# Kernel optimization log

Hardware: AMD Instinct MI355X
Metric: run time of the kernel (lower is better)

The kernel has to match this reference:

```python
import jax, jax.numpy as jnp
import numpy as np

B, S, H = 4, 2048, 1024
E, I, K = 8, 2048, 2


def setup_inputs() -> dict:
    key = jax.random.key(0)
    ks = jax.random.split(key, 6)
    return {
        "hidden_states": jax.random.normal(ks[0], (B, S, H), dtype=jnp.float32),
        "Wg": jax.random.normal(ks[1], (H, E), dtype=jnp.float32) * 0.02,
        "W1": jax.random.normal(ks[2], (E, H, I), dtype=jnp.float32) * 0.02,
        "b1": jnp.zeros((E, I), dtype=jnp.float32),
        "W2": jax.random.normal(ks[3], (E, I, H), dtype=jnp.float32) * 0.02,
        "b2": jnp.zeros((E, H), dtype=jnp.float32),
    }


def reference(hidden_states, Wg, W1, b1, W2, b2):
    b, s, h = hidden_states.shape
    x = hidden_states.reshape(-1, h)                      # [T, H]
    gate_logits = x @ Wg                                  # [T, E]
    gate_probs = jax.nn.softmax(gate_logits, axis=-1)
    topk_probs, topk_idx = jax.lax.top_k(gate_probs, K)   # [T, K]
    topk_probs = topk_probs / jnp.sum(topk_probs, axis=-1, keepdims=True)
    # dense combine weights [T, E] (zero where expert not selected)
    T = x.shape[0]
    w = jnp.zeros((T, E), dtype=x.dtype)
    w = w.at[jnp.arange(T)[:, None], topk_idx].set(topk_probs)
    # run every expert on all tokens (dense grouped-GEMM form), exact erf GELU
    h1 = jax.nn.gelu(jnp.einsum('th,ehi->eti', x, W1) + b1[:, None, :], approximate=False)  # [E, T, I]
    y = jnp.einsum('eti,eih->eth', h1, W2) + b2[:, None, :]                                  # [E, T, H]
    out = jnp.einsum('te,eth->th', w, y)                                                     # [T, H]
    return out.reshape(b, s, h)
```

## Files before the change

kernel.cpp:

```cpp
#include <hip/hip_runtime.h>
#include <math.h>

#define TOKS 8192
#define HD 1024
#define ID 2048
#define NE 8

typedef __bf16 bf16_t;
typedef __bf16 bf16x8 __attribute__((ext_vector_type(8)));
typedef float f32x4 __attribute__((ext_vector_type(4)));

#define GLOAD(gp, lp)                                                \
  __builtin_amdgcn_global_load_lds(                                  \
      (const __attribute__((address_space(1))) void*)(gp),           \
      (__attribute__((address_space(3))) void*)(lp), 16, 0, 0)

#define WAITV(N) asm volatile("s_waitcnt vmcnt(" #N ")" ::: "memory")
#define WAITL0() asm volatile("s_waitcnt lgkmcnt(0)" ::: "memory")

__device__ __forceinline__ float gelu_exact(float v) {
  const float u = v * 0.70710678118654752f;
  const float a = fabsf(u);
  const float t = 1.f / (1.f + 0.3275911f * a);
  const float poly =
      t * (0.254829592f +
           t * (-0.284496736f +
                t * (1.421413741f + t * (-1.453152027f + t * 1.061405429f))));
  float er = 1.f - poly * __expf(-a * a);
  er = copysignf(er, u);
  return 0.5f * v * (1.f + er);
}

#define WS_COUNTS 0
#define WS_OFFSETS 32
#define WS_BTOK 128
#define WS_BW (128 + 65536)
#define WS_TE (128 + 2 * 65536)
#define WS_TW (128 + 3 * 65536)
#define WS_WL 263168ull
#define WS_BLKC 266240ull
#define WS_BLKB 270336ull
#define WS_POS 274432ull
#define WS_XB 524288ull
#define WS_H1 (WS_XB + 16777216ull)
#define WS_WT (WS_H1 + 67108864ull)
#define WS_Y (WS_WT + 33554432ull)

#define MAXWL 144
#define BM 128

__global__ __launch_bounds__(256) void gate_kernel(const float* __restrict__ x,
                                                   const float* __restrict__ Wg,
                                                   bf16_t* __restrict__ xb,
                                                   int* __restrict__ tok_e,
                                                   float* __restrict__ tok_w) {
  __shared__ float WgT[NE][HD];
  const int tid = threadIdx.x;
#pragma unroll
  for (int i = 0; i < NE * HD / 256; ++i) {
    const int idx = i * 256 + tid;
    WgT[idx & 7][idx >> 3] = Wg[idx];
  }
  __syncthreads();
  const int wv = tid >> 6;
  const int lane = tid & 63;
#pragma unroll
  for (int s = 0; s < 2; ++s) {
    const int t = blockIdx.x * 8 + wv * 2 + s;
    const float* xrow = x + (size_t)t * HD;
    bf16_t* xbrow = xb + (size_t)t * HD;
    float acc[NE];
#pragma unroll
    for (int e = 0; e < NE; ++e) acc[e] = 0.f;
#pragma unroll
    for (int i = 0; i < 16; ++i) {
      const int h = i * 64 + lane;
      const float xv = xrow[h];
      xbrow[h] = (bf16_t)xv;
#pragma unroll
      for (int e = 0; e < NE; ++e) acc[e] += xv * WgT[e][h];
    }
#pragma unroll
    for (int off = 32; off >= 1; off >>= 1) {
#pragma unroll
      for (int e = 0; e < NE; ++e) acc[e] += __shfl_xor(acc[e], off);
    }
    if (lane == 0) {
      int i1 = 0;
      float l1 = acc[0];
#pragma unroll
      for (int e = 1; e < NE; ++e)
        if (acc[e] > l1) { l1 = acc[e]; i1 = e; }
      int i2 = -1;
      float l2 = -3.4e38f;
#pragma unroll
      for (int e = 0; e < NE; ++e)
        if (e != i1 && acc[e] > l2) { l2 = acc[e]; i2 = e; }
      const float q = expf(l2 - l1);
      const float w1 = 1.f / (1.f + q);
      tok_e[2 * t] = i1;
      tok_e[2 * t + 1] = i2;
      tok_w[2 * t] = w1;
      tok_w[2 * t + 1] = q * w1;
    }
  }
}

__global__ __launch_bounds__(256) void hist_kernel(const int* __restrict__ tok_e,
                                                   int* __restrict__ blk_cnt) {
  __shared__ int wcnt[4][NE];
  const int tid = threadIdx.x;
  const int idx = blockIdx.x * 256 + tid;
  const int e = tok_e[idx];
  const int w = tid >> 6;
  const int lane = tid & 63;
#pragma unroll
  for (int e0 = 0; e0 < NE; ++e0) {
    const unsigned long long m = __ballot(e == e0);
    if (lane == 0) wcnt[w][e0] = __popcll(m);
  }
  __syncthreads();
  if (tid < NE)
    blk_cnt[blockIdx.x * NE + tid] =
        wcnt[0][tid] + wcnt[1][tid] + wcnt[2][tid] + wcnt[3][tid];
}

__global__ void scan_kernel(const int* __restrict__ blk_cnt, int* __restrict__ counts,
                            int* __restrict__ offsets, int* __restrict__ blk_base,
                            int* __restrict__ wl_e, int* __restrict__ wl_m,
                            int* __restrict__ n_work) {
  const int b = threadIdx.x;
  int c[NE], pre[NE], tot[NE];
#pragma unroll
  for (int e = 0; e < NE; ++e) c[e] = blk_cnt[b * NE + e];
#pragma unroll
  for (int e = 0; e < NE; ++e) {
    int v = c[e];
#pragma unroll
    for (int off = 1; off < 64; off <<= 1) {
      const int u = __shfl_up(v, off);
      if (b >= off) v += u;
    }
    pre[e] = v - c[e];
    tot[e] = __shfl(v, 63);
  }
  int off_[NE];
  int s = 0;
#pragma unroll
  for (int e = 0; e < NE; ++e) {
    off_[e] = s;
    s += tot[e];
  }
#pragma unroll
  for (int e = 0; e < NE; ++e) blk_base[b * NE + e] = off_[e] + pre[e];
  if (b == 0) {
    int idx = 0;
    for (int e = 0; e < NE; ++e) {
      counts[e] = tot[e];
      offsets[e] = off_[e];
      for (int m = 0; m < tot[e] && idx < MAXWL; m += BM) {
        wl_e[idx] = e;
        wl_m[idx] = m;
        ++idx;
      }
    }
    *n_work = idx;
  }
}

__global__ __launch_bounds__(256) void scatter_kernel(const int* __restrict__ tok_e,
                                                      const float* __restrict__ tok_w,
                                                      const int* __restrict__ blk_base,
                                                      int* __restrict__ bucket_tok,
                                                      float* __restrict__ bucket_w,
                                                      int* __restrict__ pos_of) {
  __shared__ int wcnt[4][NE];
  const int tid = threadIdx.x;
  const int idx = blockIdx.x * 256 + tid;
  const int e = tok_e[idx];
  const int w = tid >> 6;
  const int lane = tid & 63;
  unsigned long long mym = 0;
#pragma unroll
  for (int e0 = 0; e0 < NE; ++e0) {
    const unsigned long long m = __ballot(e == e0);
    if (lane == 0) wcnt[w][e0] = __popcll(m);
    if (e0 == e) mym = m;
  }
  __syncthreads();
  int base = blk_base[blockIdx.x * NE + e];
  for (int w2 = 0; w2 < w; ++w2) base += wcnt[w2][e];
  const int rank = __popcll(mym & ((1ull << lane) - 1ull));
  const int pos = base + rank;
  bucket_tok[pos] = idx >> 1;
  bucket_w[pos] = tok_w[idx];
  pos_of[idx] = pos;
}

__global__ __launch_bounds__(256) void transpose_convert_kernel(const float* __restrict__ src,
                                                                bf16_t* __restrict__ dst, int K,
                                                                int N) {
  __shared__ float tile[64][65];
  const int e = blockIdx.z;
  const int k0 = blockIdx.x * 64;
  const int n0 = blockIdx.y * 64;
  const float* s = src + (size_t)e * K * N;
  bf16_t* d = dst + (size_t)e * K * N;
  const int t = threadIdx.x;
  const int c4 = (t & 15) * 4;
  const int rr = t >> 4;
#pragma unroll
  for (int p = 0; p < 4; ++p) {
    const int r = p * 16 + rr;
    const float4 v = *(const float4*)(s + (size_t)(k0 + r) * N + n0 + c4);
    tile[r][c4] = v.x;
    tile[r][c4 + 1] = v.y;
    tile[r][c4 + 2] = v.z;
    tile[r][c4 + 3] = v.w;
  }
  __syncthreads();
  const int kc = t & 7;
  const int nb = t >> 3;
#pragma unroll
  for (int p = 0; p < 2; ++p) {
    const int n = p * 32 + nb;
    bf16_t o[8];
#pragma unroll
    for (int j = 0; j < 8; ++j) o[j] = (bf16_t)tile[kc * 8 + j][n];
    *(uint4*)(d + (size_t)(n0 + n) * K + k0 + kc * 8) = *(uint4*)o;
  }
}


__global__ __launch_bounds__(256, 3) void gemm1_kernel(
    const bf16_t* __restrict__ xb, const bf16_t* __restrict__ W1T, const float* __restrict__ b1,
    const int* __restrict__ counts, const int* __restrict__ offsets,
    const int* __restrict__ bucket_tok, const int* __restrict__ wl_e,
    const int* __restrict__ wl_m, const int* __restrict__ n_work, bf16_t* __restrict__ h1) {
  const int widx = blockIdx.x;
  if (widx >= *n_work) return;
  const int e = wl_e[widx];
  const int m_base = wl_m[widx];
  const int n_e = counts[e];
  const int n_base = blockIdx.y * 128;
  const int off = offsets[e];

  __shared__ bf16_t As[3][128 * 32];
  __shared__ bf16_t Bs[3][128 * 32];

  const int tid = threadIdx.x;
  const int w = tid >> 6;
  const int lane = tid & 63;
  const int quad = lane >> 4;
  const int lrow = lane & 15;
  const int wm = w >> 1;
  const int wn = w & 1;

  const int srow = lane >> 2;
  const int kch = (((lane & 3) ^ ((lane >> 4) & 3)) * 8);
  int r0 = m_base + w * 32 + srow;
  int r1 = r0 + 16;
  if (r0 >= n_e) r0 = n_e - 1;
  if (r1 >= n_e) r1 = n_e - 1;
  const bf16_t* ga0 = xb + (size_t)bucket_tok[off + r0] * HD + kch;
  const bf16_t* ga1 = xb + (size_t)bucket_tok[off + r1] * HD + kch;
  const bf16_t* gb0 = W1T + ((size_t)e * ID + n_base + w * 32 + srow) * HD + kch;
  const bf16_t* gb1 = gb0 + (size_t)16 * HD;
  const int laofs0 = w * 1024 + lane * 8;
  const int laofs1 = laofs0 + 512;

  f32x4 acc[4][4];
#pragma unroll
  for (int mt = 0; mt < 4; ++mt)
#pragma unroll
    for (int nt = 0; nt < 4; ++nt)
#pragma unroll
      for (int r = 0; r < 4; ++r) acc[mt][nt][r] = 0.f;

#pragma unroll
  for (int p = 0; p < 2; ++p) {
    const size_t ko = (size_t)p * 32;
    GLOAD(ga0 + ko, &As[p][laofs0]);
    GLOAD(ga1 + ko, &As[p][laofs1]);
    GLOAD(gb0 + ko, &Bs[p][laofs0]);
    GLOAD(gb1 + ko, &Bs[p][laofs1]);
  }

  const int slot = (quad ^ ((lrow >> 2) & 3)) * 8;
  int cur = 0;
  int pre = 2;
#define NT1 (HD / 32)
  for (int kt = 0; kt < NT1; ++kt) {
    WAITL0();
    __builtin_amdgcn_s_barrier();
    if (kt + 2 < NT1) {
      const size_t ko = (size_t)(kt + 2) * 32;
      GLOAD(ga0 + ko, &As[pre][laofs0]);
      GLOAD(ga1 + ko, &As[pre][laofs1]);
      GLOAD(gb0 + ko, &Bs[pre][laofs0]);
      GLOAD(gb1 + ko, &Bs[pre][laofs1]);
      WAITV(8);
    } else if (kt + 1 < NT1) {
      WAITV(4);
    } else {
      WAITV(0);
    }
    __builtin_amdgcn_s_barrier();
    __builtin_amdgcn_sched_barrier(0);
    bf16x8 af[4], bfr[4];
#pragma unroll
    for (int i = 0; i < 4; ++i) {
      af[i] = *(const bf16x8*)(&As[cur][(wm * 64 + i * 16 + lrow) * 32 + slot]);
      bfr[i] = *(const bf16x8*)(&Bs[cur][(wn * 64 + i * 16 + lrow) * 32 + slot]);
    }
#pragma unroll
    for (int mt = 0; mt < 4; ++mt)
#pragma unroll
      for (int nt = 0; nt < 4; ++nt)
        acc[mt][nt] =
            __builtin_amdgcn_mfma_f32_16x16x32_bf16(bfr[nt], af[mt], acc[mt][nt], 0, 0, 0);
    cur = (cur == 2) ? 0 : cur + 1;
    pre = (pre == 2) ? 0 : pre + 1;
  }

#pragma unroll
  for (int mt = 0; mt < 4; ++mt) {
    const int gm = m_base + wm * 64 + mt * 16 + lrow;
    if (gm < n_e) {
      bf16_t* orow = h1 + (size_t)(off + gm) * ID;
#pragma unroll
      for (int nt = 0; nt < 4; ++nt) {
        const int gi0 = n_base + wn * 64 + nt * 16 + quad * 4;
        const float4 bb = *(const float4*)(b1 + e * ID + gi0);
        const float bv[4] = {bb.x, bb.y, bb.z, bb.w};
        bf16_t o[4];
#pragma unroll
        for (int r = 0; r < 4; ++r) o[r] = (bf16_t)gelu_exact(acc[mt][nt][r] + bv[r]);
        *(uint2*)(orow + gi0) = *(uint2*)o;
      }
    }
  }
}

__global__ __launch_bounds__(256, 3) void gemm2_kernel(
    const bf16_t* __restrict__ h1, const bf16_t* __restrict__ W2T, const float* __restrict__ b2,
    const int* __restrict__ counts, const int* __restrict__ offsets,
    const int* __restrict__ wl_e, const int* __restrict__ wl_m, const int* __restrict__ n_work,
    bf16_t* __restrict__ y) {
  const int widx = blockIdx.x;
  if (widx >= *n_work) return;
  const int e = wl_e[widx];
  const int m_base = wl_m[widx];
  const int n_e = counts[e];
  const int n_base = blockIdx.y * 128;
  const int off = offsets[e];

  __shared__ bf16_t As[3][128 * 32];
  __shared__ bf16_t Bs[3][128 * 32];

  const int tid = threadIdx.x;
  const int w = tid >> 6;
  const int lane = tid & 63;
  const int quad = lane >> 4;
  const int lrow = lane & 15;
  const int wm = w >> 1;
  const int wn = w & 1;

  const int srow = lane >> 2;
  const int kch = (((lane & 3) ^ ((lane >> 4) & 3)) * 8);
  int r0 = m_base + w * 32 + srow;
  int r1 = r0 + 16;
  if (r0 >= n_e) r0 = n_e - 1;
  if (r1 >= n_e) r1 = n_e - 1;
  const bf16_t* ga0 = h1 + (size_t)(off + r0) * ID + kch;
  const bf16_t* ga1 = h1 + (size_t)(off + r1) * ID + kch;
  const bf16_t* gb0 = W2T + ((size_t)e * HD + n_base + w * 32 + srow) * ID + kch;
  const bf16_t* gb1 = gb0 + (size_t)16 * ID;
  const int laofs0 = w * 1024 + lane * 8;
  const int laofs1 = laofs0 + 512;

  f32x4 acc[4][4];
#pragma unroll
  for (int mt = 0; mt < 4; ++mt)
#pragma unroll
    for (int nt = 0; nt < 4; ++nt)
#pragma unroll
      for (int r = 0; r < 4; ++r) acc[mt][nt][r] = 0.f;

#pragma unroll
  for (int p = 0; p < 2; ++p) {
    const size_t ko = (size_t)p * 32;
    GLOAD(ga0 + ko, &As[p][laofs0]);
    GLOAD(ga1 + ko, &As[p][laofs1]);
    GLOAD(gb0 + ko, &Bs[p][laofs0]);
    GLOAD(gb1 + ko, &Bs[p][laofs1]);
  }

  const int slot = (quad ^ ((lrow >> 2) & 3)) * 8;
  int cur = 0;
  int pre = 2;
#define NT2 (ID / 32)
  for (int kt = 0; kt < NT2; ++kt) {
    WAITL0();
    __builtin_amdgcn_s_barrier();
    if (kt + 2 < NT2) {
      const size_t ko = (size_t)(kt + 2) * 32;
      GLOAD(ga0 + ko, &As[pre][laofs0]);
      GLOAD(ga1 + ko, &As[pre][laofs1]);
      GLOAD(gb0 + ko, &Bs[pre][laofs0]);
      GLOAD(gb1 + ko, &Bs[pre][laofs1]);
      WAITV(8);
    } else if (kt + 1 < NT2) {
      WAITV(4);
    } else {
      WAITV(0);
    }
    __builtin_amdgcn_s_barrier();
    __builtin_amdgcn_sched_barrier(0);
    bf16x8 af[4], bfr[4];
#pragma unroll
    for (int i = 0; i < 4; ++i) {
      af[i] = *(const bf16x8*)(&As[cur][(wm * 64 + i * 16 + lrow) * 32 + slot]);
      bfr[i] = *(const bf16x8*)(&Bs[cur][(wn * 64 + i * 16 + lrow) * 32 + slot]);
    }
#pragma unroll
    for (int mt = 0; mt < 4; ++mt)
#pragma unroll
      for (int nt = 0; nt < 4; ++nt)
        acc[mt][nt] =
            __builtin_amdgcn_mfma_f32_16x16x32_bf16(bfr[nt], af[mt], acc[mt][nt], 0, 0, 0);
    cur = (cur == 2) ? 0 : cur + 1;
    pre = (pre == 2) ? 0 : pre + 1;
  }

#pragma unroll
  for (int mt = 0; mt < 4; ++mt) {
    const int gm = m_base + wm * 64 + mt * 16 + lrow;
    if (gm < n_e) {
      bf16_t* orow = y + (size_t)(off + gm) * HD;
#pragma unroll
      for (int nt = 0; nt < 4; ++nt) {
        const int gi0 = n_base + wn * 64 + nt * 16 + quad * 4;
        const float4 bb = *(const float4*)(b2 + e * HD + gi0);
        const float bv[4] = {bb.x, bb.y, bb.z, bb.w};
        bf16_t o[4];
#pragma unroll
        for (int r = 0; r < 4; ++r) o[r] = (bf16_t)(acc[mt][nt][r] + bv[r]);
        *(uint2*)(orow + gi0) = *(uint2*)o;
      }
    }
  }
}

__global__ __launch_bounds__(256) void combine_kernel(const bf16_t* __restrict__ y,
                                                      const int* __restrict__ pos_of,
                                                      const float* __restrict__ tok_w,
                                                      float* __restrict__ out) {
  const int gid = blockIdx.x * 256 + threadIdx.x;
  const int t = gid >> 7;
  const int c8 = (gid & 127) * 8;
  const int p1 = pos_of[2 * t];
  const int p2 = pos_of[2 * t + 1];
  const float w1 = tok_w[2 * t];
  const float w2 = tok_w[2 * t + 1];
  const bf16x8 a = *(const bf16x8*)(y + (size_t)p1 * HD + c8);
  const bf16x8 b = *(const bf16x8*)(y + (size_t)p2 * HD + c8);
  float* op = out + (size_t)t * HD + c8;
  float ov[8];
#pragma unroll
  for (int j = 0; j < 8; ++j) ov[j] = w1 * (float)a[j] + w2 * (float)b[j];
  *(float4*)op = make_float4(ov[0], ov[1], ov[2], ov[3]);
  *(float4*)(op + 4) = make_float4(ov[4], ov[5], ov[6], ov[7]);
}

extern "C" void kernel_launch(void* const* d_in, const int* in_sizes, int n_in,
                              void* d_out, int out_size, void* d_ws, size_t ws_size,
                              hipStream_t stream) {
  const float* x = (const float*)d_in[0];
  const float* Wg = (const float*)d_in[1];
  const float* W1 = (const float*)d_in[2];
  const float* b1 = (const float*)d_in[3];
  const float* W2 = (const float*)d_in[4];
  const float* b2 = (const float*)d_in[5];
  float* out = (float*)d_out;
  char* ws = (char*)d_ws;

  int* counts = (int*)(ws + WS_COUNTS);
  int* offsets = (int*)(ws + WS_OFFSETS);
  int* bucket_tok = (int*)(ws + WS_BTOK);
  float* bucket_w = (float*)(ws + WS_BW);
  int* tok_e = (int*)(ws + WS_TE);
  float* tok_w = (float*)(ws + WS_TW);
  int* wl_e = (int*)(ws + WS_WL);
  int* wl_m = wl_e + MAXWL;
  int* n_work = wl_m + MAXWL;
  int* blk_cnt = (int*)(ws + WS_BLKC);
  int* blk_base = (int*)(ws + WS_BLKB);
  int* pos_of = (int*)(ws + WS_POS);
  bf16_t* xb = (bf16_t*)(ws + WS_XB);
  bf16_t* h1 = (bf16_t*)(ws + WS_H1);
  bf16_t* WT = (bf16_t*)(ws + WS_WT);
  bf16_t* y = (bf16_t*)(ws + WS_Y);

  gate_kernel<<<TOKS / 8, 256, 0, stream>>>(x, Wg, xb, tok_e, tok_w);
  hist_kernel<<<TOKS * 2 / 256, 256, 0, stream>>>(tok_e, blk_cnt);
  scan_kernel<<<1, 64, 0, stream>>>(blk_cnt, counts, offsets, blk_base, wl_e, wl_m, n_work);
  scatter_kernel<<<TOKS * 2 / 256, 256, 0, stream>>>(tok_e, tok_w, blk_base, bucket_tok,
                                                     bucket_w, pos_of);
  transpose_convert_kernel<<<dim3(HD / 64, ID / 64, NE), 256, 0, stream>>>(W1, WT, HD, ID);
  gemm1_kernel<<<dim3(MAXWL, ID / 128), 256, 0, stream>>>(xb, WT, b1, counts, offsets, bucket_tok,
                                                          wl_e, wl_m, n_work, h1);
  transpose_convert_kernel<<<dim3(ID / 64, HD / 64, NE), 256, 0, stream>>>(W2, WT, ID, HD);
  gemm2_kernel<<<dim3(MAXWL, HD / 128), 256, 0, stream>>>(h1, WT, b2, counts, offsets, wl_e,
                                                          wl_m, n_work, y);
  combine_kernel<<<TOKS * HD / (256 * 8), 256, 0, stream>>>(y, pos_of, tok_w, out);
}
```

Measured before the change: 447.8 us.

## Fuse expert histogram into gate kernel, vectorize gate weights, raise MFMA priority

The gate kernel now counts per-block expert assignments with shared-memory atomics and records each slot's local rank, which removes the separate histogram kernel launch. The scan kernel is extended to handle 1024 gate blocks (16 per lane), and the scatter kernel uses the precomputed ranks in place of ballots. Gate weights are kept in their natural [H,E] layout and read as float4 pairs. The GEMM inner loops also wrap the MFMA block in s_setprio to favour the math waves. Atomic ranks make bucket order within an expert nondeterministic, and the scan does more serial work per thread.

```diff
diff --git a/kernel.cpp b/kernel.cpp
--- a/kernel.cpp
+++ b/kernel.cpp
@@ -38,9 +38,10 @@
 #define WS_TE (128 + 2 * 65536)
 #define WS_TW (128 + 3 * 65536)
 #define WS_WL 263168ull
-#define WS_BLKC 266240ull
-#define WS_BLKB 270336ull
 #define WS_POS 274432ull
+#define WS_RANK 339968ull
+#define WS_BLKC 405504ull
+#define WS_BLKB 438272ull
 #define WS_XB 524288ull
 #define WS_H1 (WS_XB + 16777216ull)
 #define WS_WT (WS_H1 + 67108864ull)
@@ -48,19 +49,24 @@
 
 #define MAXWL 144
 #define BM 128
+#define GB (TOKS / 8)
 
 __global__ __launch_bounds__(256) void gate_kernel(const float* __restrict__ x,
                                                    const float* __restrict__ Wg,
                                                    bf16_t* __restrict__ xb,
                                                    int* __restrict__ tok_e,
-                                                   float* __restrict__ tok_w) {
-  __shared__ float WgT[NE][HD];
+                                                   float* __restrict__ tok_w,
+                                                   int* __restrict__ rank_of,
+                                                   int* __restrict__ blk_cnt) {
+  __shared__ float WgT[HD * NE];
+  __shared__ int cnt[NE];
   const int tid = threadIdx.x;
 #pragma unroll
-  for (int i = 0; i < NE * HD / 256; ++i) {
-    const int idx = i * 256 + tid;
-    WgT[idx & 7][idx >> 3] = Wg[idx];
-  }
+  for (int i = 0; i < NE * HD / (256 * 4); ++i) {
+    const int k = i * 256 + tid;
+    ((float4*)WgT)[k] = ((const float4*)Wg)[k];
+  }
+  if (tid < NE) cnt[tid] = 0;
   __syncthreads();
   const int wv = tid >> 6;
   const int lane = tid & 63;
@@ -77,8 +83,16 @@
       const int h = i * 64 + lane;
       const float xv = xrow[h];
       xbrow[h] = (bf16_t)xv;
-#pragma unroll
-      for (int e = 0; e < NE; ++e) acc[e] += xv * WgT[e][h];
+      const float4 w0 = *(const float4*)(WgT + h * NE);
+      const float4 w1 = *(const float4*)(WgT + h * NE + 4);
+      acc[0] += xv * w0.x;
+      acc[1] += xv * w0.y;
+      acc[2] += xv * w0.z;
+      acc[3] += xv * w0.w;
+      acc[4] += xv * w1.x;
+      acc[5] += xv * w1.y;
+      acc[6] += xv * w1.z;
+      acc[7] += xv * w1.w;
     }
 #pragma unroll
     for (int off = 32; off >= 1; off >>= 1) {
@@ -102,27 +116,12 @@
       tok_e[2 * t + 1] = i2;
       tok_w[2 * t] = w1;
       tok_w[2 * t + 1] = q * w1;
-    }
-  }
-}
-
-__global__ __launch_bounds__(256) void hist_kernel(const int* __restrict__ tok_e,
-                                                   int* __restrict__ blk_cnt) {
-  __shared__ int wcnt[4][NE];
-  const int tid = threadIdx.x;
-  const int idx = blockIdx.x * 256 + tid;
-  const int e = tok_e[idx];
-  const int w = tid >> 6;
-  const int lane = tid & 63;
-#pragma unroll
-  for (int e0 = 0; e0 < NE; ++e0) {
-    const unsigned long long m = __ballot(e == e0);
-    if (lane == 0) wcnt[w][e0] = __popcll(m);
+      rank_of[2 * t] = atomicAdd(&cnt[i1], 1);
+      rank_of[2 * t + 1] = atomicAdd(&cnt[i2], 1);
+    }
   }
   __syncthreads();
-  if (tid < NE)
-    blk_cnt[blockIdx.x * NE + tid] =
-        wcnt[0][tid] + wcnt[1][tid] + wcnt[2][tid] + wcnt[3][tid];
+  if (tid < NE) blk_cnt[blockIdx.x * NE + tid] = cnt[tid];
 }
 
 __global__ void scan_kernel(const int* __restrict__ blk_cnt, int* __restrict__ counts,
@@ -130,18 +129,22 @@
                             int* __restrict__ wl_e, int* __restrict__ wl_m,
                             int* __restrict__ n_work) {
   const int b = threadIdx.x;
-  int c[NE], pre[NE], tot[NE];
-#pragma unroll
-  for (int e = 0; e < NE; ++e) c[e] = blk_cnt[b * NE + e];
+  int sum[NE], pre[NE], tot[NE];
 #pragma unroll
   for (int e = 0; e < NE; ++e) {
-    int v = c[e];
+    int s = 0;
+    for (int j = 0; j < 16; ++j) s += blk_cnt[(b * 16 + j) * NE + e];
+    sum[e] = s;
+  }
+#pragma unroll
+  for (int e = 0; e < NE; ++e) {
+    int v = sum[e];
 #pragma unroll
     for (int off = 1; off < 64; off <<= 1) {
       const int u = __shfl_up(v, off);
       if (b >= off) v += u;
     }
-    pre[e] = v - c[e];
+    pre[e] = v - sum[e];
     tot[e] = __shfl(v, 63);
   }
   int off_[NE];
@@ -152,7 +155,13 @@
     s += tot[e];
   }
 #pragma unroll
-  for (int e = 0; e < NE; ++e) blk_base[b * NE + e] = off_[e] + pre[e];
+  for (int e = 0; e < NE; ++e) {
+    int run = off_[e] + pre[e];
+    for (int j = 0; j < 16; ++j) {
+      blk_base[(b * 16 + j) * NE + e] = run;
+      run += blk_cnt[(b * 16 + j) * NE + e];
+    }
+  }
   if (b == 0) {
     int idx = 0;
     for (int e = 0; e < NE; ++e) {
@@ -171,27 +180,14 @@
 __global__ __launch_bounds__(256) void scatter_kernel(const int* __restrict__ tok_e,
                                                       const float* __restrict__ tok_w,
                                                       const int* __restrict__ blk_base,
+                                                      const int* __restrict__ rank_of,
                                                       int* __restrict__ bucket_tok,
                                                       float* __restrict__ bucket_w,
                                                       int* __restrict__ pos_of) {
-  __shared__ int wcnt[4][NE];
-  const int tid = threadIdx.x;
-  const int idx = blockIdx.x * 256 + tid;
+  const int idx = blockIdx.x * 256 + threadIdx.x;
   const int e = tok_e[idx];
-  const int w = tid >> 6;
-  const int lane = tid & 63;
-  unsigned long long mym = 0;
-#pragma unroll
-  for (int e0 = 0; e0 < NE; ++e0) {
-    const unsigned long long m = __ballot(e == e0);
-    if (lane == 0) wcnt[w][e0] = __popcll(m);
-    if (e0 == e) mym = m;
-  }
-  __syncthreads();
-  int base = blk_base[blockIdx.x * NE + e];
-  for (int w2 = 0; w2 < w; ++w2) base += wcnt[w2][e];
-  const int rank = __popcll(mym & ((1ull << lane) - 1ull));
-  const int pos = base + rank;
+  const int gb = idx >> 4;
+  const int pos = blk_base[gb * NE + e] + rank_of[idx];
   bucket_tok[pos] = idx >> 1;
   bucket_w[pos] = tok_w[idx];
   pos_of[idx] = pos;
@@ -313,12 +309,14 @@
       af[i] = *(const bf16x8*)(&As[cur][(wm * 64 + i * 16 + lrow) * 32 + slot]);
       bfr[i] = *(const bf16x8*)(&Bs[cur][(wn * 64 + i * 16 + lrow) * 32 + slot]);
     }
+    __builtin_amdgcn_s_setprio(1);
 #pragma unroll
     for (int mt = 0; mt < 4; ++mt)
 #pragma unroll
       for (int nt = 0; nt < 4; ++nt)
         acc[mt][nt] =
             __builtin_amdgcn_mfma_f32_16x16x32_bf16(bfr[nt], af[mt], acc[mt][nt], 0, 0, 0);
+    __builtin_amdgcn_s_setprio(0);
     cur = (cur == 2) ? 0 : cur + 1;
     pre = (pre == 2) ? 0 : pre + 1;
   }
@@ -423,12 +421,14 @@
       af[i] = *(const bf16x8*)(&As[cur][(wm * 64 + i * 16 + lrow) * 32 + slot]);
       bfr[i] = *(const bf16x8*)(&Bs[cur][(wn * 64 + i * 16 + lrow) * 32 + slot]);
     }
+    __builtin_amdgcn_s_setprio(1);
 #pragma unroll
     for (int mt = 0; mt < 4; ++mt)
 #pragma unroll
       for (int nt = 0; nt < 4; ++nt)
         acc[mt][nt] =
             __builtin_amdgcn_mfma_f32_16x16x32_bf16(bfr[nt], af[mt], acc[mt][nt], 0, 0, 0);
+    __builtin_amdgcn_s_setprio(0);
     cur = (cur == 2) ? 0 : cur + 1;
     pre = (pre == 2) ? 0 : pre + 1;
   }
@@ -494,19 +494,19 @@
   int* wl_e = (int*)(ws + WS_WL);
   int* wl_m = wl_e + MAXWL;
   int* n_work = wl_m + MAXWL;
+  int* pos_of = (int*)(ws + WS_POS);
+  int* rank_of = (int*)(ws + WS_RANK);
   int* blk_cnt = (int*)(ws + WS_BLKC);
   int* blk_base = (int*)(ws + WS_BLKB);
-  int* pos_of = (int*)(ws + WS_POS);
   bf16_t* xb = (bf16_t*)(ws + WS_XB);
   bf16_t* h1 = (bf16_t*)(ws + WS_H1);
   bf16_t* WT = (bf16_t*)(ws + WS_WT);
   bf16_t* y = (bf16_t*)(ws + WS_Y);
 
-  gate_kernel<<<TOKS / 8, 256, 0, stream>>>(x, Wg, xb, tok_e, tok_w);
-  hist_kernel<<<TOKS * 2 / 256, 256, 0, stream>>>(tok_e, blk_cnt);
+  gate_kernel<<<GB, 256, 0, stream>>>(x, Wg, xb, tok_e, tok_w, rank_of, blk_cnt);
   scan_kernel<<<1, 64, 0, stream>>>(blk_cnt, counts, offsets, blk_base, wl_e, wl_m, n_work);
-  scatter_kernel<<<TOKS * 2 / 256, 256, 0, stream>>>(tok_e, tok_w, blk_base, bucket_tok,
-                                                     bucket_w, pos_of);
+  scatter_kernel<<<TOKS * 2 / 256, 256, 0, stream>>>(tok_e, tok_w, blk_base, rank_of,
+                                                     bucket_tok, bucket_w, pos_of);
   transpose_convert_kernel<<<dim3(HD / 64, ID / 64, NE), 256, 0, stream>>>(W1, WT, HD, ID);
   gemm1_kernel<<<dim3(MAXWL, ID / 128), 256, 0, stream>>>(xb, WT, b1, counts, offsets, bucket_tok,
                                                           wl_e, wl_m, n_work, h1);
```

Result: no change. 447.4 us (-0.1%).
